# Kernel tuning notes

Measured on AMD Instinct MI355X. Metric: run time of the kernel, lower is better.

## Reference

```python
import jax, jax.numpy as jnp
import numpy as np


def setup_inputs() -> dict:
    key = jax.random.key(0)
    k1, k2 = jax.random.split(key)
    B, C, KX, KZ = 512, 256, 6, 22
    x = jax.random.normal(k1, (B, C, KX, KX), dtype=jnp.float32)  # exemplar (kernel)
    z = jax.random.normal(k2, (B, C, KZ, KZ), dtype=jnp.float32)  # search region (input)
    return {"x": x, "z": z}


def reference(x, z):
    # Per-sample cross-correlation: out[b] = conv2d(z[b], x[b]) (valid, stride 1).
    # Expressed as a single grouped convolution with groups=B instead of a
    # Python loop of B separate conv2d calls.
    B, C, kz, _ = z.shape
    z2 = z.reshape(1, B * C, kz, kz)              # [1, B*C, kz, kz]
    out = jax.lax.conv_general_dilated(
        z2, x,
        window_strides=(1, 1),
        padding="VALID",
        dimension_numbers=("NCHW", "OIHW", "NCHW"),
        feature_group_count=B,
    )                                              # [1, B, ho, wo]
    return jnp.transpose(out, (1, 0, 2, 3))        # [B, 1, ho, wo]
```

## Files before the change

kernel.cpp:

```cpp
#include <hip/hip_runtime.h>
#include <cstdint>
#include <cstddef>

#define BB      512
#define CC      256
#define KXX     6
#define KZZ     22
#define HO      17
#define OUTHW   (HO * HO)
#define ZCH     (KZZ * KZZ)
#define XCH     (KXX * KXX)

#define CHUNK_C   8
#define NCHUNK    (CC / CHUNK_C)
#define ZCHUNK    (CHUNK_C * ZCH)
#define XCHUNK    (CHUNK_C * XCH)
#define NT        320
#define NW        5

typedef const __attribute__((address_space(1))) void* gptr_t;
typedef __attribute__((address_space(3))) void* lptr_t;

__device__ __forceinline__ void cp16_async(void* lds_base, const void* gsrc) {
  __builtin_amdgcn_global_load_lds((gptr_t)gsrc, (lptr_t)lds_base, 16, 0, 0);
}
__device__ __forceinline__ void cp4_async(void* lds_base, const void* gsrc) {
  __builtin_amdgcn_global_load_lds((gptr_t)gsrc, (lptr_t)lds_base, 4, 0, 0);
}

__device__ __forceinline__ void stage_chunk(float* zdst, float* xdst,
                                            const float* zsrc, const float* xsrc,
                                            int wave, int lane) {
  char* zd = (char*)zdst;
  const char* zs = (const char*)zsrc;
#pragma unroll
  for (int i = 0; i < 3; ++i) {
    const int grp = wave * 3 + i;
    cp16_async(zd + grp * 1024, zs + grp * 1024 + lane * 16);
  }
  if (wave == 0) {
    if (lane < 32) cp4_async(zd + 15360, zs + 15360 + lane * 4);
  } else if (wave == 1) {
    cp16_async((char*)xdst, (const char*)xsrc + lane * 16);
  } else if (wave == 2) {
    if (lane < 32) cp4_async((char*)xdst + 1024, (const char*)xsrc + 1024 + lane * 4);
  }
}

__global__ __launch_bounds__(NT, 2) void corr_kernel(const float* __restrict__ x,
                                                     const float* __restrict__ z,
                                                     float* __restrict__ out) {
  __shared__ __align__(16) float zbuf[2][ZCHUNK];
  __shared__ __align__(16) float xbuf[2][XCHUNK];

  const int b    = blockIdx.x;
  const int t    = threadIdx.x;
  const int wave = t >> 6;
  const int lane = t & 63;

  const float* zb = z + (size_t)b * (CC * ZCH);
  const float* xb = x + (size_t)b * (CC * XCH);

  stage_chunk(zbuf[0], xbuf[0], zb, xb, wave, lane);

  const int  g      = t / 17;
  const int  oy     = t - g * 17;
  const int  cl     = g & 7;
  const int  kyh    = g >> 3;
  const bool active = (g < 16);

  float acc[HO];
#pragma unroll
  for (int i = 0; i < HO; ++i) acc[i] = 0.0f;

  for (int k = 0; k < NCHUNK; ++k) {
    const int buf = k & 1;
    __syncthreads();

    if (k + 1 < NCHUNK)
      stage_chunk(zbuf[buf ^ 1], xbuf[buf ^ 1],
                  zb + (size_t)(k + 1) * ZCHUNK, xb + (size_t)(k + 1) * XCHUNK,
                  wave, lane);

    if (active) {
      const float* zc = &zbuf[buf][cl * ZCH];
      const float* xc = &xbuf[buf][cl * XCH + kyh * (3 * KXX)];

      __align__(16) float xv[3 * KXX];
#pragma unroll
      for (int i = 0; i < 9; ++i)
        ((float2*)xv)[i] = ((const float2*)xc)[i];

#pragma unroll
      for (int ky2 = 0; ky2 < 3; ++ky2) {
        const int row = oy + kyh * 3 + ky2;
        const float* zr = zc + row * KZZ;
        __align__(16) float zv[KZZ + 1];
#pragma unroll
        for (int i = 0; i < 11; ++i)
          ((float2*)zv)[i] = ((const float2*)zr)[i];
#pragma unroll
        for (int kx = 0; kx < KXX; ++kx) {
          const float xs = xv[ky2 * KXX + kx];
#pragma unroll
          for (int ox = 0; ox < HO; ++ox)
            acc[ox] = fmaf(zv[ox + kx], xs, acc[ox]);
        }
      }
    }
  }

  __syncthreads();
  float* red = &zbuf[0][0];
  if (active) {
#pragma unroll
    for (int ox = 0; ox < HO; ++ox)
      red[g * OUTHW + oy * HO + ox] = acc[ox];
  }
  __syncthreads();
  if (t < OUTHW) {
    float s = 0.0f;
#pragma unroll
    for (int gg = 0; gg < 16; ++gg) s += red[gg * OUTHW + t];
    out[(size_t)b * OUTHW + t] = s;
  }
}

extern "C" void kernel_launch(void* const* d_in, const int* in_sizes, int n_in,
                              void* d_out, int out_size, void* d_ws, size_t ws_size,
                              hipStream_t stream) {
  const float* x = (const float*)d_in[0];
  const float* z = (const float*)d_in[1];
  float* out = (float*)d_out;
  corr_kernel<<<BB, NT, 0, stream>>>(x, z, out);
}
```

Baseline: 360.9 us.

## Deepen LDS staging to triple buffering with explicit vmcnt waits

The kernel moves from double to triple buffering of the z/x chunks in LDS. It prefetches two chunks ahead and replaces __syncthreads with an explicit s_waitcnt vmcnt(4) plus a raw s_barrier. Each wave now issues exactly four async loads per stage (a dummy scratch load was added to balance the count), so the vmcnt accounting allows one chunk to remain in flight. The extra buffer raises LDS usage, which may limit occupancy at 2 blocks per CU. Correctness depends on the hand-counted vmcnt matching the loads the compiler actually emits.

```diff
diff --git a/kernel.cpp b/kernel.cpp
--- a/kernel.cpp
+++ b/kernel.cpp
@@ -15,8 +15,8 @@
 #define NCHUNK    (CC / CHUNK_C)
 #define ZCHUNK    (CHUNK_C * ZCH)
 #define XCHUNK    (CHUNK_C * XCH)
+#define NBUF      3
 #define NT        320
-#define NW        5
 
 typedef const __attribute__((address_space(1))) void* gptr_t;
 typedef __attribute__((address_space(3))) void* lptr_t;
@@ -29,6 +29,7 @@
 }
 
 __device__ __forceinline__ void stage_chunk(float* zdst, float* xdst,
+                                            float* scratch,
                                             const float* zsrc, const float* xsrc,
                                             int wave, int lane) {
   char* zd = (char*)zdst;
@@ -44,14 +45,23 @@
     cp16_async((char*)xdst, (const char*)xsrc + lane * 16);
   } else if (wave == 2) {
     if (lane < 32) cp4_async((char*)xdst + 1024, (const char*)xsrc + 1024 + lane * 4);
+  } else {
+    if (lane < 32) cp4_async((char*)scratch, zs + lane * 4);
   }
+}
+
+__device__ __forceinline__ void pipe_barrier() {
+  asm volatile("" ::: "memory");
+  __builtin_amdgcn_s_barrier();
+  asm volatile("" ::: "memory");
 }
 
 __global__ __launch_bounds__(NT, 2) void corr_kernel(const float* __restrict__ x,
                                                      const float* __restrict__ z,
                                                      float* __restrict__ out) {
-  __shared__ __align__(16) float zbuf[2][ZCHUNK];
-  __shared__ __align__(16) float xbuf[2][XCHUNK];
+  __shared__ __align__(16) float zbuf[NBUF][ZCHUNK];
+  __shared__ __align__(16) float xbuf[NBUF][XCHUNK];
+  __shared__ __align__(16) float scratch[32];
 
   const int b    = blockIdx.x;
   const int t    = threadIdx.x;
@@ -61,7 +71,8 @@
   const float* zb = z + (size_t)b * (CC * ZCH);
   const float* xb = x + (size_t)b * (CC * XCH);
 
-  stage_chunk(zbuf[0], xbuf[0], zb, xb, wave, lane);
+  stage_chunk(zbuf[0], xbuf[0], scratch, zb, xb, wave, lane);
+  stage_chunk(zbuf[1], xbuf[1], scratch, zb + ZCHUNK, xb + XCHUNK, wave, lane);
 
   const int  g      = t / 17;
   const int  oy     = t - g * 17;
@@ -74,15 +85,22 @@
   for (int i = 0; i < HO; ++i) acc[i] = 0.0f;
 
   for (int k = 0; k < NCHUNK; ++k) {
-    const int buf = k & 1;
-    __syncthreads();
+    if (k < NCHUNK - 1) {
+      asm volatile("s_waitcnt vmcnt(4)" ::: "memory");
+    } else {
+      asm volatile("s_waitcnt vmcnt(0)" ::: "memory");
+    }
+    pipe_barrier();
 
-    if (k + 1 < NCHUNK)
-      stage_chunk(zbuf[buf ^ 1], xbuf[buf ^ 1],
-                  zb + (size_t)(k + 1) * ZCHUNK, xb + (size_t)(k + 1) * XCHUNK,
+    if (k + 2 < NCHUNK) {
+      const int nb = (k + 2) % NBUF;
+      stage_chunk(zbuf[nb], xbuf[nb], scratch,
+                  zb + (size_t)(k + 2) * ZCHUNK, xb + (size_t)(k + 2) * XCHUNK,
                   wave, lane);
+    }
 
     if (active) {
+      const int buf = k % NBUF;
       const float* zc = &zbuf[buf][cl * ZCH];
       const float* xc = &xbuf[buf][cl * XCH + kyh * (3 * KXX)];
 
@@ -95,7 +113,7 @@
       for (int ky2 = 0; ky2 < 3; ++ky2) {
         const int row = oy + kyh * 3 + ky2;
         const float* zr = zc + row * KZZ;
-        __align__(16) float zv[KZZ + 1];
+        __align__(16) float zv[KZZ + 2];
 #pragma unroll
         for (int i = 0; i < 11; ++i)
           ((float2*)zv)[i] = ((const float2*)zr)[i];
```

After: 399.9 us. +10.8%, slower.

## Compute two output rows per thread over 16-channel chunks, read kernel from global

Applied to the files above, without the earlier changes.

Doubles the channel chunk to 16 and remaps threads so each computes two adjacent output rows, reusing each loaded z row for both accumulators. The exemplar weights are now read straight from global/L2 into registers instead of being staged in LDS, and staging becomes uniform 16-byte copies. This cuts LDS read traffic per FMA and halves the number of barriers, at the cost of doubled accumulator registers, which may lower occupancy under the launch bounds, plus uncoalesced global loads for weights.

```diff
diff --git a/kernel.cpp b/kernel.cpp
--- a/kernel.cpp
+++ b/kernel.cpp
@@ -11,12 +11,10 @@
 #define ZCH     (KZZ * KZZ)
 #define XCH     (KXX * KXX)
 
-#define CHUNK_C   8
+#define CHUNK_C   16
 #define NCHUNK    (CC / CHUNK_C)
 #define ZCHUNK    (CHUNK_C * ZCH)
-#define XCHUNK    (CHUNK_C * XCH)
 #define NT        320
-#define NW        5
 
 typedef const __attribute__((address_space(1))) void* gptr_t;
 typedef __attribute__((address_space(3))) void* lptr_t;
@@ -24,34 +22,24 @@
 __device__ __forceinline__ void cp16_async(void* lds_base, const void* gsrc) {
   __builtin_amdgcn_global_load_lds((gptr_t)gsrc, (lptr_t)lds_base, 16, 0, 0);
 }
-__device__ __forceinline__ void cp4_async(void* lds_base, const void* gsrc) {
-  __builtin_amdgcn_global_load_lds((gptr_t)gsrc, (lptr_t)lds_base, 4, 0, 0);
-}
 
-__device__ __forceinline__ void stage_chunk(float* zdst, float* xdst,
-                                            const float* zsrc, const float* xsrc,
+__device__ __forceinline__ void stage_chunk(float* zdst, const float* zsrc,
                                             int wave, int lane) {
   char* zd = (char*)zdst;
   const char* zs = (const char*)zsrc;
 #pragma unroll
-  for (int i = 0; i < 3; ++i) {
-    const int grp = wave * 3 + i;
+  for (int i = 0; i < 6; ++i) {
+    const int grp = wave * 6 + i;
     cp16_async(zd + grp * 1024, zs + grp * 1024 + lane * 16);
   }
-  if (wave == 0) {
-    if (lane < 32) cp4_async(zd + 15360, zs + 15360 + lane * 4);
-  } else if (wave == 1) {
-    cp16_async((char*)xdst, (const char*)xsrc + lane * 16);
-  } else if (wave == 2) {
-    if (lane < 32) cp4_async((char*)xdst + 1024, (const char*)xsrc + 1024 + lane * 4);
-  }
+  if (wave == 0 && lane < 16)
+    cp16_async(zd + 30720, zs + 30720 + lane * 16);
 }
 
 __global__ __launch_bounds__(NT, 2) void corr_kernel(const float* __restrict__ x,
                                                      const float* __restrict__ z,
                                                      float* __restrict__ out) {
   __shared__ __align__(16) float zbuf[2][ZCHUNK];
-  __shared__ __align__(16) float xbuf[2][XCHUNK];
 
   const int b    = blockIdx.x;
   const int t    = threadIdx.x;
@@ -61,50 +49,62 @@
   const float* zb = z + (size_t)b * (CC * ZCH);
   const float* xb = x + (size_t)b * (CC * XCH);
 
-  stage_chunk(zbuf[0], xbuf[0], zb, xb, wave, lane);
+  stage_chunk(zbuf[0], zb, wave, lane);
 
-  const int  g      = t / 17;
-  const int  oy     = t - g * 17;
-  const int  cl     = g & 7;
-  const int  kyh    = g >> 3;
-  const bool active = (g < 16);
+  const int  g2     = t / 9;
+  const int  oyg    = t - g2 * 9;
+  const int  cl     = g2 >> 1;
+  const int  kyh    = g2 & 1;
+  const bool active = (t < 288);
+  const bool two    = (oyg < 8);
 
-  float acc[HO];
+  float acc0[HO], acc1[HO];
 #pragma unroll
-  for (int i = 0; i < HO; ++i) acc[i] = 0.0f;
+  for (int i = 0; i < HO; ++i) { acc0[i] = 0.0f; acc1[i] = 0.0f; }
 
   for (int k = 0; k < NCHUNK; ++k) {
     const int buf = k & 1;
     __syncthreads();
 
     if (k + 1 < NCHUNK)
-      stage_chunk(zbuf[buf ^ 1], xbuf[buf ^ 1],
-                  zb + (size_t)(k + 1) * ZCHUNK, xb + (size_t)(k + 1) * XCHUNK,
-                  wave, lane);
+      stage_chunk(zbuf[buf ^ 1], zb + (size_t)(k + 1) * ZCHUNK, wave, lane);
 
     if (active) {
+      const float* xs = xb + ((size_t)(k * CHUNK_C + cl)) * XCH + kyh * 18;
+      float xv[18];
+#pragma unroll
+      for (int j = 0; j < 9; ++j)
+        ((float2*)xv)[j] = ((const float2*)xs)[j];
+
       const float* zc = &zbuf[buf][cl * ZCH];
-      const float* xc = &xbuf[buf][cl * XCH + kyh * (3 * KXX)];
-
-      __align__(16) float xv[3 * KXX];
-#pragma unroll
-      for (int i = 0; i < 9; ++i)
-        ((float2*)xv)[i] = ((const float2*)xc)[i];
+      const int base_row = 2 * oyg + 3 * kyh;
 
 #pragma unroll
-      for (int ky2 = 0; ky2 < 3; ++ky2) {
-        const int row = oy + kyh * 3 + ky2;
-        const float* zr = zc + row * KZZ;
-        __align__(16) float zv[KZZ + 1];
+      for (int ri = 0; ri < 4; ++ri) {
+        if (ri < 3 || two) {
+          const float* zr = zc + (base_row + ri) * KZZ;
+          float zv[KZZ + 2];
 #pragma unroll
-        for (int i = 0; i < 11; ++i)
-          ((float2*)zv)[i] = ((const float2*)zr)[i];
+          for (int i = 0; i < 11; ++i)
+            ((float2*)zv)[i] = ((const float2*)zr)[i];
+          if (ri <= 2) {
 #pragma unroll
-        for (int kx = 0; kx < KXX; ++kx) {
-          const float xs = xv[ky2 * KXX + kx];
+            for (int kx = 0; kx < KXX; ++kx) {
+              const float xs0 = xv[ri * KXX + kx];
 #pragma unroll
-          for (int ox = 0; ox < HO; ++ox)
-            acc[ox] = fmaf(zv[ox + kx], xs, acc[ox]);
+              for (int ox = 0; ox < HO; ++ox)
+                acc0[ox] = fmaf(zv[ox + kx], xs0, acc0[ox]);
+            }
+          }
+          if (ri >= 1 && two) {
+#pragma unroll
+            for (int kx = 0; kx < KXX; ++kx) {
+              const float xs1 = xv[(ri - 1) * KXX + kx];
+#pragma unroll
+              for (int ox = 0; ox < HO; ++ox)
+                acc1[ox] = fmaf(zv[ox + kx], xs1, acc1[ox]);
+            }
+          }
         }
       }
     }
@@ -113,15 +113,21 @@
   __syncthreads();
   float* red = &zbuf[0][0];
   if (active) {
+    const int oy0 = 2 * oyg;
 #pragma unroll
     for (int ox = 0; ox < HO; ++ox)
-      red[g * OUTHW + oy * HO + ox] = acc[ox];
+      red[g2 * OUTHW + oy0 * HO + ox] = acc0[ox];
+    if (two) {
+#pragma unroll
+      for (int ox = 0; ox < HO; ++ox)
+        red[g2 * OUTHW + (oy0 + 1) * HO + ox] = acc1[ox];
+    }
   }
   __syncthreads();
   if (t < OUTHW) {
     float s = 0.0f;
 #pragma unroll
-    for (int gg = 0; gg < 16; ++gg) s += red[gg * OUTHW + t];
+    for (int gg = 0; gg < 32; ++gg) s += red[gg * OUTHW + t];
     out[(size_t)b * OUTHW + t] = s;
   }
 }
```

Measured after the change: 381.9 us. +5.8%, slower.
